# Performance work log

Measured on AMD Instinct MI355X. Metric: run time of the kernel, lower is better.

The kernel has to match this reference:

```python
import jax, jax.numpy as jnp
import numpy as np
from jax import lax

E = 1e-13            # WENO smoothness epsilon
MULT_BIAS = 0.1      # weno5_mult_bias
PADS = (2, 2, 0, 0, 1, 0)


def _conv1d(x, w, b, pad):
    # x: [1, Cin, N], w: [Cout, Cin, K], b: [Cout]
    y = lax.conv_general_dilated(x, w, window_strides=(1,), padding=[(pad, pad)],
                                 dimension_numbers=('NCH', 'OIH', 'NCH'))
    return y + b[None, :, None]


def _cnn(dif, params):
    # inner_nn_weno5: 5 Conv+ELU blocks then Conv+Sigmoid; dif: [N]
    x = dif[None, None, :]
    for i in range(6):
        x = _conv1d(x, params[2 * i], params[2 * i + 1], PADS[i])
        x = jax.nn.elu(x) if i < 5 else jax.nn.sigmoid(x)
    return x[0, 0]  # [N]


def _avg_diff(uu):
    # __get_average_diff: average of left/right forward differences, edges replicated
    d = uu[1:] - uu[:-1]                       # [N-1]
    d_left = jnp.concatenate([d, d[-1:]])      # [N]
    d_right = jnp.concatenate([d[:1], d])      # [N]
    return 0.5 * (d_left + d_right)


def _weno5(uu, params):
    # w5_minus=True, mweno=True, mapped=False, trainable=True
    def fluxes(u):
        um, umm = jnp.roll(u, 1), jnp.roll(u, 2)
        up, upp = jnp.roll(u, -1), jnp.roll(u, -2)
        f0 = (11 * u - 7 * up + 2 * upp) / 6
        f1 = (2 * um + 5 * u - up) / 6
        f2 = (-umm + 5 * um + 2 * u) / 6
        return f0, f1, f2

    def betas(u):
        um, umm = jnp.roll(u, 1), jnp.roll(u, 2)
        up, upp = jnp.roll(u, -1), jnp.roll(u, -2)
        b0 = 13 / 12 * (u - 2 * up + upp) ** 2 + 0.25 * (3 * u - 4 * up + upp) ** 2
        b1 = 13 / 12 * (um - 2 * u + up) ** 2 + 0.25 * (um - up) ** 2
        b2 = 13 / 12 * (umm - 2 * um + u) ** 2 + 0.25 * (umm - 4 * um + 3 * u) ** 2
        return b0, b1, b2

    u_right = jnp.roll(uu, -1)
    fp = fluxes(u_right)
    fn = fluxes(uu)
    bp = list(betas(u_right))
    bn = list(betas(uu))

    # trainable beta correction from the small CNN flux limiter
    bm = _cnn(_avg_diff(uu), params) + MULT_BIAS
    bp = [b * jnp.roll(bm, k - 1) for k, b in enumerate(bp)]
    bn = [b * jnp.roll(bm, k - 1) for k, b in enumerate(bn)]

    ds = (0.1, 0.6, 0.3)

    def omegas(bs):  # mweno=True variant, then normalize
        brs = (bs[2] - bs[0]) ** 2
        om = [d / (E + b) ** 2 * (brs + (E + b) ** 2) for b, d in zip(bs, ds)]
        s = om[0] + om[1] + om[2]
        return [o / s for o in om]

    op = omegas(bp)
    on = omegas(bn)
    fluxp = op[0] * fp[0] + op[1] * fp[1] + op[2] * fp[2]
    fluxn = on[0] * fn[0] + on[1] * fn[1] + on[2] * fn[2]
    return fluxp - fluxn


def setup_inputs() -> dict:
    key = jax.random.key(0)
    ks = jax.random.split(key, 13)
    N = 2097152
    uu = jax.random.normal(ks[0], (N,), dtype=jnp.float32)
    shapes = [(20, 1, 5), (40, 20, 5), (80, 40, 1), (40, 80, 1), (20, 40, 3), (1, 20, 1)]
    inp = {'uu': uu}
    for i, (co, ci, k) in enumerate(shapes):
        fan_in = ci * k
        scale = jnp.float32(1.0 / np.sqrt(fan_in))
        inp[f'w{i + 1}'] = jax.random.normal(ks[2 * i + 1], (co, ci, k), dtype=jnp.float32) * scale
        inp[f'b{i + 1}'] = jax.random.normal(ks[2 * i + 2], (co,), dtype=jnp.float32) * 0.01
    return inp


def reference(uu, w1, b1, w2, b2, w3, b3, w4, b4, w5, b5, w6, b6):
    params = (w1, b1, w2, b2, w3, b3, w4, b4, w5, b5, w6, b6)
    return _weno5(uu, params)
```

## Files before the change

kernel.cpp:

```cpp
#include <hip/hip_runtime.h>
#include <cstdint>

#define N_PTS 2097152
#define MASK  (N_PTS - 1)

constexpr int NPOS = 128;
constexpr int POUT = 116;
constexpr int GOFF = 6;
constexpr int BLK  = 256;
constexpr int NBLK = (N_PTS + POUT - 1) / POUT;

constexpr int ST1 = 40;
constexpr int ST2 = 72;
constexpr int ST3 = 104;
constexpr int ST4 = 72;

constexpr int SLOTA_OFF = 0;
constexpr int SLOTA_SZ  = 128 * ST3 * 2;
constexpr int SLOTB_OFF = SLOTA_SZ;
constexpr int SLOTB_SZ  = 130 * ST4 * 2;
constexpr int TAIL_OFF  = SLOTB_OFF + SLOTB_SZ;
constexpr int SMEM_BYTES = TAIL_OFF + 392 * 4;

constexpr int F2 = 0;
constexpr int F3 = 7680;
constexpr int F4 = 12800;
constexpr int F5 = 17408;
constexpr int F1 = 23552;
constexpr int NFRAG2 = 15, NFRAG3 = 10, NFRAG4 = 9, NFRAG5 = 12;
constexpr int NPREP = NFRAG2 + NFRAG3 + NFRAG4 + NFRAG5 + 2;
constexpr int BME_OFF = 65536;

typedef __bf16 bf16x8 __attribute__((ext_vector_type(8)));
typedef unsigned short u16x8 __attribute__((ext_vector_type(8)));
typedef float f32x4 __attribute__((ext_vector_type(4)));

constexpr unsigned short BF16_ONE = 0x3F80;

__device__ __forceinline__ float elu(float x) { return x > 0.f ? x : __expf(x) - 1.f; }

__device__ __forceinline__ float fastrcp(float x) {
#if __has_builtin(__builtin_amdgcn_rcpf)
    return __builtin_amdgcn_rcpf(x);
#else
    return 1.f / x;
#endif
}

__device__ __forceinline__ unsigned short f2b_rtne(float f) {
    union { float f; unsigned int u; } x; x.f = f;
    return (unsigned short)((x.u + 0x7fffu + ((x.u >> 16) & 1u)) >> 16);
}
__device__ __forceinline__ unsigned int pack_bf16_2(float lo, float hi) {
#if __has_builtin(__builtin_amdgcn_perm)
    union { float f; unsigned int u; } a, b;
    a.f = lo; b.f = hi;
    return __builtin_amdgcn_perm(b.u + 0x8000u, a.u + 0x8000u, 0x07060302u);
#else
    union { float f; unsigned int u; } a, b;
    a.f = lo; b.f = hi;
    return ((a.u + 0x8000u) >> 16) | (((b.u + 0x8000u) >> 16) << 16);
#endif
}

template<int M, int MT, int CI, int KS, int KT>
__device__ __forceinline__ void pack_one(const float* __restrict__ W,
                                         const float* __restrict__ Bias, int biasTap,
                                         unsigned short* __restrict__ dst,
                                         int f, int lane)
{
    const int ks = f % KS;
    const int fi = f / KS;
    const int mt = fi % MT;
    const int t  = fi / MT;
    const int m  = mt * 16 + (lane & 15);
    const int kb = ks * 32 + (lane >> 4) * 8;
    u16x8 v;
    #pragma unroll
    for (int j = 0; j < 8; ++j) {
        const int k = kb + j;
        float val = 0.f;
        if (m < M) {
            if (k < CI)                          val = W[(m * CI + k) * KT + t];
            else if (k == CI && t == biasTap)    val = Bias[m];
        }
        v[j] = f2b_rtne(val);
    }
    *(u16x8*)(dst + (f * 64 + lane) * 8) = v;
}

__global__ __launch_bounds__(64) void prep_kernel(
    const float* __restrict__ w1, const float* __restrict__ b1,
    const float* __restrict__ w2, const float* __restrict__ b2,
    const float* __restrict__ w3, const float* __restrict__ b3,
    const float* __restrict__ w4, const float* __restrict__ b4,
    const float* __restrict__ w5, const float* __restrict__ b5,
    unsigned short* __restrict__ frags)
{
    const int lane = threadIdx.x;
    const int b = blockIdx.x;
    if (b < NFRAG2)
        pack_one<40, 3, 20, 1, 5>(w2, b2, 2, frags + F2, b, lane);
    else if (b < NFRAG2 + NFRAG3)
        pack_one<80, 5, 40, 2, 1>(w3, b3, 0, frags + F3, b - NFRAG2, lane);
    else if (b < NFRAG2 + NFRAG3 + NFRAG4)
        pack_one<40, 3, 80, 3, 1>(w4, b4, 0, frags + F4, b - NFRAG2 - NFRAG3, lane);
    else if (b < NFRAG2 + NFRAG3 + NFRAG4 + NFRAG5)
        pack_one<20, 2, 40, 2, 3>(w5, b5, 1, frags + F5, b - NFRAG2 - NFRAG3 - NFRAG4, lane);
    else {
        const int mt = b - (NPREP - 2);
        const int m  = mt * 16 + (lane & 15);
        const int kb = (lane >> 4) * 8;
        u16x8 v;
        #pragma unroll
        for (int j = 0; j < 8; ++j) {
            const int k = kb + j;
            float val = 0.f;
            if (m < 20) {
                if (k < 5)      val = w1[m * 5 + k];
                else if (k == 5) val = b1[m];
            }
            v[j] = f2b_rtne(val);
        }
        *(u16x8*)(frags + F1 + (mt * 64 + lane) * 8) = v;
    }
}

template<int TAPS, int MT, int KS, typename Epi>
__device__ __forceinline__ void gemm_tap(const unsigned short* __restrict__ Af,
                                         const unsigned short* __restrict__ Bbuf,
                                         int SB, Epi epi)
{
    const int lane = threadIdx.x & 63;
    const int wv   = threadIdx.x >> 6;
    const int n15  = lane & 15;
    const int quad = lane >> 4;

    bf16x8 A[TAPS * MT * KS];
    #pragma unroll
    for (int f = 0; f < TAPS * MT * KS; ++f)
        A[f] = __builtin_bit_cast(bf16x8, *(const u16x8*)(Af + (f * 64 + lane) * 8));

    #pragma unroll
    for (int nt = 0; nt < 2; ++nt) {
        const int pos = (wv * 2 + nt) * 16 + n15;
        bf16x8 B[TAPS][KS];
        #pragma unroll
        for (int t = 0; t < TAPS; ++t)
            #pragma unroll
            for (int ks = 0; ks < KS; ++ks)
                B[t][ks] = __builtin_bit_cast(bf16x8,
                    *(const u16x8*)(Bbuf + (pos + t) * SB + ks * 32 + quad * 8));
        #pragma unroll
        for (int mt = 0; mt < MT; ++mt) {
            f32x4 acc = {0.f, 0.f, 0.f, 0.f};
            #pragma unroll
            for (int t = 0; t < TAPS; ++t)
                #pragma unroll
                for (int ks = 0; ks < KS; ++ks)
                    acc = __builtin_amdgcn_mfma_f32_16x16x32_bf16(
                        A[(t * MT + mt) * KS + ks], B[t][ks], acc, 0, 0, 0);
            epi(mt, pos, acc);
        }
    }
}

__device__ __forceinline__ float weno_math(float um2, float um1, float u0,
                                           float up1, float up2, float up3,
                                           float bmm, float bm0, float bmp)
{
    const float c1312 = 13.f / 12.f;
    const float s6 = 1.f / 6.f;

    const float f0p = (11.f * up1 - 7.f * up2 + 2.f * up3) * s6;
    const float f1p = (2.f * u0 + 5.f * up1 - up2) * s6;
    const float f2p = (-um1 + 5.f * u0 + 2.f * up1) * s6;
    const float f0n = (11.f * u0 - 7.f * up1 + 2.f * up2) * s6;
    const float f1n = (2.f * um1 + 5.f * u0 - up1) * s6;
    const float f2n = (-um2 + 5.f * um1 + 2.f * u0) * s6;

    float t0, t1;
    t0 = up1 - 2.f * up2 + up3;  t1 = 3.f * up1 - 4.f * up2 + up3;
    float bp0 = c1312 * t0 * t0 + 0.25f * t1 * t1;
    t0 = u0 - 2.f * up1 + up2;   t1 = u0 - up2;
    float bp1 = c1312 * t0 * t0 + 0.25f * t1 * t1;
    t0 = um1 - 2.f * u0 + up1;   t1 = um1 - 4.f * u0 + 3.f * up1;
    float bp2 = c1312 * t0 * t0 + 0.25f * t1 * t1;
    t0 = u0 - 2.f * up1 + up2;   t1 = 3.f * u0 - 4.f * up1 + up2;
    float bn0 = c1312 * t0 * t0 + 0.25f * t1 * t1;
    t0 = um1 - 2.f * u0 + up1;   t1 = um1 - up1;
    float bn1 = c1312 * t0 * t0 + 0.25f * t1 * t1;
    t0 = um2 - 2.f * um1 + u0;   t1 = um2 - 4.f * um1 + 3.f * u0;
    float bn2 = c1312 * t0 * t0 + 0.25f * t1 * t1;

    bp0 *= bmp; bp1 *= bm0; bp2 *= bmm;
    bn0 *= bmp; bn1 *= bm0; bn2 *= bmm;

    const float E = 1e-13f;
    float brs, e, r0, r1, r2, o0, o1, o2;

    brs = bp2 - bp0; brs *= brs;
    e = E + bp0; e *= e; r0 = fastrcp(e);
    e = E + bp1; e *= e; r1 = fastrcp(e);
    e = E + bp2; e *= e; r2 = fastrcp(e);
    o0 = 0.1f * fmaf(brs, r0, 1.f);
    o1 = 0.6f * fmaf(brs, r1, 1.f);
    o2 = 0.3f * fmaf(brs, r2, 1.f);
    const float fluxp = (o0 * f0p + o1 * f1p + o2 * f2p) * fastrcp(o0 + o1 + o2);

    brs = bn2 - bn0; brs *= brs;
    e = E + bn0; e *= e; r0 = fastrcp(e);
    e = E + bn1; e *= e; r1 = fastrcp(e);
    e = E + bn2; e *= e; r2 = fastrcp(e);
    o0 = 0.1f * fmaf(brs, r0, 1.f);
    o1 = 0.6f * fmaf(brs, r1, 1.f);
    o2 = 0.3f * fmaf(brs, r2, 1.f);
    const float fluxn = (o0 * f0n + o1 * f1n + o2 * f2n) * fastrcp(o0 + o1 + o2);

    return fluxp - fluxn;
}

__global__ __launch_bounds__(BLK, 3) void cnn_weno_kernel(
    const float* __restrict__ u,
    const float* __restrict__ w6, const float* __restrict__ b6,
    const unsigned short* __restrict__ frags,
    float* __restrict__ bmE,
    float* __restrict__ out)
{
    extern __shared__ char smem[];
    unsigned short* act1 = (unsigned short*)(smem + SLOTA_OFF);
    unsigned short* act3 = (unsigned short*)(smem + SLOTA_OFF);
    unsigned short* act2 = (unsigned short*)(smem + SLOTB_OFF);
    unsigned short* act4 = (unsigned short*)(smem + SLOTB_OFF);
    float* sdif = (float*)(smem + TAIL_OFF);
    float* sw6  = sdif + 132;
    float* sb6  = sw6 + 20;
    float* sbm  = sb6 + 1;
    float* su   = sbm + 118;

    const int tid  = threadIdx.x;
    const int lane = tid & 63;
    const int wv   = tid >> 6;
    const int n15  = lane & 15;
    const int quad = lane >> 4;
    const int i0   = blockIdx.x * POUT;
    const bool edge = (blockIdx.x == 0) || (blockIdx.x >= NBLK - 1);

    {
        const u16x8 z8 = {0, 0, 0, 0, 0, 0, 0, 0};
        for (int i = tid; i < 130 * 2; i += BLK) {
            const int r = i >> 1, c = 48 + (i & 1) * 8;
            *(u16x8*)(act2 + r * ST2 + c) = z8;
        }
        for (int i = tid; i < 128 * 2; i += BLK) {
            const int r = i >> 1, j = i & 1;
            u16x8 v = {0, 0, 0, 0, 0, 0, 0, 0};
            if (j == 0) v[0] = BF16_ONE;
            *(u16x8*)(act3 + r * ST3 + 80 + j * 8) = v;
        }
    }
    for (int d = tid; d < 132; d += BLK) {
        const int g = i0 - 10 + d;
        float v = 0.f;
        if (g >= 0 && g < N_PTS) {
            if (g == 0)              v = u[1] - u[0];
            else if (g == N_PTS - 1) v = u[N_PTS - 1] - u[N_PTS - 2];
            else                     v = 0.5f * (u[g + 1] - u[g - 1]);
        }
        sdif[d] = v;
    }
    for (int j = tid; j < 121; j += BLK)
        su[j] = u[(i0 - 2 + j) & MASK];
    if (tid < 20)       sw6[tid] = w6[tid];
    else if (tid == 20) sb6[0] = b6[0];
    __syncthreads();

    {
        bf16x8 A1[2];
        #pragma unroll
        for (int f = 0; f < 2; ++f)
            A1[f] = __builtin_bit_cast(bf16x8,
                *(const u16x8*)(frags + F1 + (f * 64 + lane) * 8));
        #pragma unroll
        for (int nt = 0; nt < 2; ++nt) {
            const int pos = (wv * 2 + nt) * 16 + n15;
            const float s0 = sdif[pos],     s1 = sdif[pos + 1], s2 = sdif[pos + 2],
                        s3 = sdif[pos + 3], s4 = sdif[pos + 4];
            uint4 bd;
            bd.x = pack_bf16_2(s0, s1);
            bd.y = pack_bf16_2(s2, s3);
            bd.z = pack_bf16_2(s4, 1.0f);
            bd.w = 0u;
            const bf16x8 B = __builtin_bit_cast(bf16x8, bd);
            const f32x4 z = {0.f, 0.f, 0.f, 0.f};
            const f32x4 a0 = __builtin_amdgcn_mfma_f32_16x16x32_bf16(A1[0], B, z, 0, 0, 0);
            const f32x4 a1 = __builtin_amdgcn_mfma_f32_16x16x32_bf16(A1[1], B, z, 0, 0, 0);
            bool oor = false;
            if (edge) {
                const int g = i0 + pos - 8;
                oor = ((unsigned)g >= (unsigned)N_PTS);
            }
            {
                float v0 = elu(a0[0]), v1 = elu(a0[1]), v2 = elu(a0[2]), v3 = elu(a0[3]);
                if (oor) { v0 = v1 = v2 = v3 = 0.f; }
                uint2 w; w.x = pack_bf16_2(v0, v1); w.y = pack_bf16_2(v2, v3);
                *(uint2*)(act1 + pos * ST1 + quad * 4) = w;
            }
            {
                uint2 w;
                if (quad == 0) {
                    float v0 = elu(a1[0]), v1 = elu(a1[1]), v2 = elu(a1[2]), v3 = elu(a1[3]);
                    if (oor) { v0 = v1 = v2 = v3 = 0.f; }
                    w.x = pack_bf16_2(v0, v1); w.y = pack_bf16_2(v2, v3);
                } else if (quad == 1) {
                    w.x = (unsigned)BF16_ONE; w.y = 0u;
                } else {
                    w.x = 0u; w.y = 0u;
                }
                *(uint2*)(act1 + pos * ST1 + 16 + quad * 4) = w;
            }
        }
    }
    __syncthreads();

    gemm_tap<5, 3, 1>(frags + F2, act1, ST1,
        [&](int mt, int pos, f32x4 acc) {
            const int ch0 = mt * 16 + quad * 4;
            unsigned short* dst = act2 + pos * ST2 + ch0;
            if (mt < 2 || quad < 2) {
                float v0 = elu(acc[0]), v1 = elu(acc[1]), v2 = elu(acc[2]), v3 = elu(acc[3]);
                if (edge) {
                    const int g = i0 - GOFF + pos;
                    if ((unsigned)g >= (unsigned)N_PTS) { v0 = v1 = v2 = v3 = 0.f; }
                }
                uint2 w; w.x = pack_bf16_2(v0, v1); w.y = pack_bf16_2(v2, v3);
                *(uint2*)dst = w;
            } else {
                uint2 w; w.x = (quad == 2) ? (unsigned)BF16_ONE : 0u; w.y = 0u;
                *(uint2*)dst = w;
            }
        });
    __syncthreads();

    gemm_tap<1, 5, 2>(frags + F3, act2, ST2,
        [&](int mt, int pos, f32x4 acc) {
            const int ch0 = mt * 16 + quad * 4;
            float v0 = elu(acc[0]), v1 = elu(acc[1]), v2 = elu(acc[2]), v3 = elu(acc[3]);
            if (edge) {
                const int g = i0 - GOFF + pos;
                if ((unsigned)g >= (unsigned)N_PTS) { v0 = v1 = v2 = v3 = 0.f; }
            }
            uint2 w; w.x = pack_bf16_2(v0, v1); w.y = pack_bf16_2(v2, v3);
            *(uint2*)(act3 + pos * ST3 + ch0) = w;
        });
    __syncthreads();

    gemm_tap<1, 3, 3>(frags + F4, act3, ST3,
        [&](int mt, int pos, f32x4 acc) {
            const int ch0 = mt * 16 + quad * 4;
            unsigned short* dst = act4 + (pos + 1) * ST4 + ch0;
            if (mt < 2 || quad < 2) {
                float v0 = elu(acc[0]), v1 = elu(acc[1]), v2 = elu(acc[2]), v3 = elu(acc[3]);
                if (edge) {
                    const int g = i0 - GOFF + pos;
                    if ((unsigned)g >= (unsigned)N_PTS) { v0 = v1 = v2 = v3 = 0.f; }
                }
                uint2 w; w.x = pack_bf16_2(v0, v1); w.y = pack_bf16_2(v2, v3);
                *(uint2*)dst = w;
            } else {
                uint2 w; w.x = (quad == 2) ? (unsigned)BF16_ONE : 0u; w.y = 0u;
                *(uint2*)dst = w;
            }
        });
    __syncthreads();

    {
        const unsigned short* Af = frags + F5;
        bf16x8 A5[12];
        #pragma unroll
        for (int f = 0; f < 12; ++f)
            A5[f] = __builtin_bit_cast(bf16x8, *(const u16x8*)(Af + (f * 64 + lane) * 8));

        #pragma unroll
        for (int nt = 0; nt < 2; ++nt) {
            const int pos = (wv * 2 + nt) * 16 + n15;
            bf16x8 B[3][2];
            #pragma unroll
            for (int t = 0; t < 3; ++t)
                #pragma unroll
                for (int ks = 0; ks < 2; ++ks)
                    B[t][ks] = __builtin_bit_cast(bf16x8,
                        *(const u16x8*)(act4 + (pos + t) * ST4 + ks * 32 + quad * 8));
            f32x4 a0 = {0.f, 0.f, 0.f, 0.f};
            f32x4 a1 = {0.f, 0.f, 0.f, 0.f};
            #pragma unroll
            for (int t = 0; t < 3; ++t)
                #pragma unroll
                for (int ks = 0; ks < 2; ++ks) {
                    a0 = __builtin_amdgcn_mfma_f32_16x16x32_bf16(
                        A5[(t * 2 + 0) * 2 + ks], B[t][ks], a0, 0, 0, 0);
                    a1 = __builtin_amdgcn_mfma_f32_16x16x32_bf16(
                        A5[(t * 2 + 1) * 2 + ks], B[t][ks], a1, 0, 0, 0);
                }
            float partial = 0.f;
            const int c0 = quad * 4;
            #pragma unroll
            for (int r = 0; r < 4; ++r)
                partial += sw6[c0 + r] * elu(a0[r]);
            if (quad == 0) {
                #pragma unroll
                for (int r = 0; r < 4; ++r)
                    partial += sw6[16 + r] * elu(a1[r]);
            }
            partial += __shfl_xor(partial, 16, 64);
            partial += __shfl_xor(partial, 32, 64);
            if (quad == 0) {
                const float bmv = fastrcp(1.f + __expf(-(partial + sb6[0]))) + 0.1f;
                if (pos >= 5 && pos < 123) sbm[pos - 5] = bmv;
                if (edge) {
                    const int g = i0 - GOFF + pos;
                    if (blockIdx.x == 0) {
                        if (g == 0) bmE[0] = bmv;
                        else if (g == 1) bmE[1] = bmv;
                    }
                    if (blockIdx.x == NBLK - 1) {
                        if (g == N_PTS - 2) bmE[2] = bmv;
                        else if (g == N_PTS - 1) bmE[3] = bmv;
                    }
                }
            }
        }
    }
    __syncthreads();

    if (tid < POUT) {
        const int g = i0 + tid;
        if (g < N_PTS && g != 0 && g != N_PTS - 1) {
            out[g] = weno_math(su[tid], su[tid + 1], su[tid + 2],
                               su[tid + 3], su[tid + 4], su[tid + 5],
                               sbm[tid], sbm[tid + 1], sbm[tid + 2]);
        }
    }
}

__global__ __launch_bounds__(64) void patch_kernel(
    const float* __restrict__ u, const float* __restrict__ bmE,
    float* __restrict__ out)
{
    const int t = threadIdx.x;
    if (t < 2) {
        const int g = (t == 0) ? 0 : (N_PTS - 1);
        const float bmm = (t == 0) ? bmE[3] : bmE[2];
        const float bm0 = (t == 0) ? bmE[0] : bmE[3];
        const float bmp = (t == 0) ? bmE[1] : bmE[0];
        out[g] = weno_math(u[(g - 2) & MASK], u[(g - 1) & MASK], u[g],
                           u[(g + 1) & MASK], u[(g + 2) & MASK], u[(g + 3) & MASK],
                           bmm, bm0, bmp);
    }
}

extern "C" void kernel_launch(void* const* d_in, const int* in_sizes, int n_in,
                              void* d_out, int out_size, void* d_ws, size_t ws_size,
                              hipStream_t stream) {
    const float* u  = (const float*)d_in[0];
    const float* w1 = (const float*)d_in[1];
    const float* b1 = (const float*)d_in[2];
    const float* w2 = (const float*)d_in[3];
    const float* b2 = (const float*)d_in[4];
    const float* w3 = (const float*)d_in[5];
    const float* b3 = (const float*)d_in[6];
    const float* w4 = (const float*)d_in[7];
    const float* b4 = (const float*)d_in[8];
    const float* w5 = (const float*)d_in[9];
    const float* b5 = (const float*)d_in[10];
    const float* w6 = (const float*)d_in[11];
    const float* b6 = (const float*)d_in[12];

    unsigned short* frags = (unsigned short*)d_ws;
    float* bmE = (float*)((char*)d_ws + BME_OFF);

    (void)hipFuncSetAttribute((const void*)cnn_weno_kernel,
                              hipFuncAttributeMaxDynamicSharedMemorySize,
                              SMEM_BYTES);

    prep_kernel<<<NPREP, 64, 0, stream>>>(w1, b1, w2, b2, w3, b3, w4, b4, w5, b5, frags);
    cnn_weno_kernel<<<NBLK, BLK, SMEM_BYTES, stream>>>(u, w6, b6, frags, bmE,
                                                       (float*)d_out);
    patch_kernel<<<1, 64, 0, stream>>>(u, bmE, (float*)d_out);
}
```

Baseline: 299.4 us.

## Fold edge patch into main kernel via last-block atomic counter

Removes the separate patch kernel launch: each block bumps a global counter after finishing, and the last block computes the two periodic edge outputs from the stored boundary bm values. It also splits the halo loading into a fast path without bounds checks for interior blocks, and seeds each MFMA accumulation chain with a shared zero vector instead of a fresh zero initialiser. The exchange is one extra atomic and a __syncthreads per block, plus a __threadfence on the edge writers.

```diff
diff --git a/kernel.cpp b/kernel.cpp
--- a/kernel.cpp
+++ b/kernel.cpp
@@ -95,10 +95,12 @@
     const float* __restrict__ w3, const float* __restrict__ b3,
     const float* __restrict__ w4, const float* __restrict__ b4,
     const float* __restrict__ w5, const float* __restrict__ b5,
-    unsigned short* __restrict__ frags)
+    unsigned short* __restrict__ frags,
+    unsigned int* __restrict__ counter)
 {
     const int lane = threadIdx.x;
     const int b = blockIdx.x;
+    if (b == 0 && lane == 0) counter[0] = 0u;
     if (b < NFRAG2)
         pack_one<40, 3, 20, 1, 5>(w2, b2, 2, frags + F2, b, lane);
     else if (b < NFRAG2 + NFRAG3)
@@ -129,7 +131,7 @@
 template<int TAPS, int MT, int KS, typename Epi>
 __device__ __forceinline__ void gemm_tap(const unsigned short* __restrict__ Af,
                                          const unsigned short* __restrict__ Bbuf,
-                                         int SB, Epi epi)
+                                         int SB, f32x4 Z4, Epi epi)
 {
     const int lane = threadIdx.x & 63;
     const int wv   = threadIdx.x >> 6;
@@ -153,13 +155,14 @@
                     *(const u16x8*)(Bbuf + (pos + t) * SB + ks * 32 + quad * 8));
         #pragma unroll
         for (int mt = 0; mt < MT; ++mt) {
-            f32x4 acc = {0.f, 0.f, 0.f, 0.f};
+            f32x4 acc = __builtin_amdgcn_mfma_f32_16x16x32_bf16(
+                A[mt * KS], B[0][0], Z4, 0, 0, 0);
             #pragma unroll
-            for (int t = 0; t < TAPS; ++t)
-                #pragma unroll
-                for (int ks = 0; ks < KS; ++ks)
-                    acc = __builtin_amdgcn_mfma_f32_16x16x32_bf16(
-                        A[(t * MT + mt) * KS + ks], B[t][ks], acc, 0, 0, 0);
+            for (int i = 1; i < TAPS * KS; ++i) {
+                const int t = i / KS, ks = i - t * KS;
+                acc = __builtin_amdgcn_mfma_f32_16x16x32_bf16(
+                    A[(t * MT + mt) * KS + ks], B[t][ks], acc, 0, 0, 0);
+            }
             epi(mt, pos, acc);
         }
     }
@@ -225,6 +228,7 @@
     const float* __restrict__ w6, const float* __restrict__ b6,
     const unsigned short* __restrict__ frags,
     float* __restrict__ bmE,
+    unsigned int* __restrict__ counter,
     float* __restrict__ out)
 {
     extern __shared__ char smem[];
@@ -246,6 +250,8 @@
     const int i0   = blockIdx.x * POUT;
     const bool edge = (blockIdx.x == 0) || (blockIdx.x >= NBLK - 1);
 
+    const f32x4 Z4 = {0.f, 0.f, 0.f, 0.f};
+
     {
         const u16x8 z8 = {0, 0, 0, 0, 0, 0, 0, 0};
         for (int i = tid; i < 130 * 2; i += BLK) {
@@ -259,18 +265,27 @@
             *(u16x8*)(act3 + r * ST3 + 80 + j * 8) = v;
         }
     }
-    for (int d = tid; d < 132; d += BLK) {
-        const int g = i0 - 10 + d;
-        float v = 0.f;
-        if (g >= 0 && g < N_PTS) {
-            if (g == 0)              v = u[1] - u[0];
-            else if (g == N_PTS - 1) v = u[N_PTS - 1] - u[N_PTS - 2];
-            else                     v = 0.5f * (u[g + 1] - u[g - 1]);
-        }
-        sdif[d] = v;
-    }
-    for (int j = tid; j < 121; j += BLK)
-        su[j] = u[(i0 - 2 + j) & MASK];
+    if (!edge) {
+        for (int d = tid; d < 132; d += BLK) {
+            const int g = i0 - 10 + d;
+            sdif[d] = 0.5f * (u[g + 1] - u[g - 1]);
+        }
+        for (int j = tid; j < 121; j += BLK)
+            su[j] = u[i0 - 2 + j];
+    } else {
+        for (int d = tid; d < 132; d += BLK) {
+            const int g = i0 - 10 + d;
+            float v = 0.f;
+            if (g >= 0 && g < N_PTS) {
+                if (g == 0)              v = u[1] - u[0];
+                else if (g == N_PTS - 1) v = u[N_PTS - 1] - u[N_PTS - 2];
+                else                     v = 0.5f * (u[g + 1] - u[g - 1]);
+            }
+            sdif[d] = v;
+        }
+        for (int j = tid; j < 121; j += BLK)
+            su[j] = u[(i0 - 2 + j) & MASK];
+    }
     if (tid < 20)       sw6[tid] = w6[tid];
     else if (tid == 20) sb6[0] = b6[0];
     __syncthreads();
@@ -292,9 +307,8 @@
             bd.z = pack_bf16_2(s4, 1.0f);
             bd.w = 0u;
             const bf16x8 B = __builtin_bit_cast(bf16x8, bd);
-            const f32x4 z = {0.f, 0.f, 0.f, 0.f};
-            const f32x4 a0 = __builtin_amdgcn_mfma_f32_16x16x32_bf16(A1[0], B, z, 0, 0, 0);
-            const f32x4 a1 = __builtin_amdgcn_mfma_f32_16x16x32_bf16(A1[1], B, z, 0, 0, 0);
+            const f32x4 a0 = __builtin_amdgcn_mfma_f32_16x16x32_bf16(A1[0], B, Z4, 0, 0, 0);
+            const f32x4 a1 = __builtin_amdgcn_mfma_f32_16x16x32_bf16(A1[1], B, Z4, 0, 0, 0);
             bool oor = false;
             if (edge) {
                 const int g = i0 + pos - 8;
@@ -323,7 +337,7 @@
     }
     __syncthreads();
 
-    gemm_tap<5, 3, 1>(frags + F2, act1, ST1,
+    gemm_tap<5, 3, 1>(frags + F2, act1, ST1, Z4,
         [&](int mt, int pos, f32x4 acc) {
             const int ch0 = mt * 16 + quad * 4;
             unsigned short* dst = act2 + pos * ST2 + ch0;
@@ -342,7 +356,7 @@
         });
     __syncthreads();
 
-    gemm_tap<1, 5, 2>(frags + F3, act2, ST2,
+    gemm_tap<1, 5, 2>(frags + F3, act2, ST2, Z4,
         [&](int mt, int pos, f32x4 acc) {
             const int ch0 = mt * 16 + quad * 4;
             float v0 = elu(acc[0]), v1 = elu(acc[1]), v2 = elu(acc[2]), v3 = elu(acc[3]);
@@ -355,7 +369,7 @@
         });
     __syncthreads();
 
-    gemm_tap<1, 3, 3>(frags + F4, act3, ST3,
+    gemm_tap<1, 3, 3>(frags + F4, act3, ST3, Z4,
         [&](int mt, int pos, f32x4 acc) {
             const int ch0 = mt * 16 + quad * 4;
             unsigned short* dst = act4 + (pos + 1) * ST4 + ch0;
@@ -391,17 +405,16 @@
                 for (int ks = 0; ks < 2; ++ks)
                     B[t][ks] = __builtin_bit_cast(bf16x8,
                         *(const u16x8*)(act4 + (pos + t) * ST4 + ks * 32 + quad * 8));
-            f32x4 a0 = {0.f, 0.f, 0.f, 0.f};
-            f32x4 a1 = {0.f, 0.f, 0.f, 0.f};
+            f32x4 a0 = __builtin_amdgcn_mfma_f32_16x16x32_bf16(A5[0], B[0][0], Z4, 0, 0, 0);
+            f32x4 a1 = __builtin_amdgcn_mfma_f32_16x16x32_bf16(A5[2], B[0][0], Z4, 0, 0, 0);
             #pragma unroll
-            for (int t = 0; t < 3; ++t)
-                #pragma unroll
-                for (int ks = 0; ks < 2; ++ks) {
-                    a0 = __builtin_amdgcn_mfma_f32_16x16x32_bf16(
-                        A5[(t * 2 + 0) * 2 + ks], B[t][ks], a0, 0, 0, 0);
-                    a1 = __builtin_amdgcn_mfma_f32_16x16x32_bf16(
-                        A5[(t * 2 + 1) * 2 + ks], B[t][ks], a1, 0, 0, 0);
-                }
+            for (int i = 1; i < 6; ++i) {
+                const int t = i >> 1, ks = i & 1;
+                a0 = __builtin_amdgcn_mfma_f32_16x16x32_bf16(
+                    A5[(t * 2 + 0) * 2 + ks], B[t][ks], a0, 0, 0, 0);
+                a1 = __builtin_amdgcn_mfma_f32_16x16x32_bf16(
+                    A5[(t * 2 + 1) * 2 + ks], B[t][ks], a1, 0, 0, 0);
+            }
             float partial = 0.f;
             const int c0 = quad * 4;
             #pragma unroll
@@ -419,14 +432,16 @@
                 if (pos >= 5 && pos < 123) sbm[pos - 5] = bmv;
                 if (edge) {
                     const int g = i0 - GOFF + pos;
+                    bool wrote = false;
                     if (blockIdx.x == 0) {
-                        if (g == 0) bmE[0] = bmv;
-                        else if (g == 1) bmE[1] = bmv;
+                        if (g == 0)      { bmE[0] = bmv; wrote = true; }
+                        else if (g == 1) { bmE[1] = bmv; wrote = true; }
                     }
                     if (blockIdx.x == NBLK - 1) {
-                        if (g == N_PTS - 2) bmE[2] = bmv;
-                        else if (g == N_PTS - 1) bmE[3] = bmv;
+                        if (g == N_PTS - 2)      { bmE[2] = bmv; wrote = true; }
+                        else if (g == N_PTS - 1) { bmE[3] = bmv; wrote = true; }
                     }
+                    if (wrote) __threadfence();
                 }
             }
         }
@@ -441,21 +456,19 @@
                                sbm[tid], sbm[tid + 1], sbm[tid + 2]);
         }
     }
-}
-
-__global__ __launch_bounds__(64) void patch_kernel(
-    const float* __restrict__ u, const float* __restrict__ bmE,
-    float* __restrict__ out)
-{
-    const int t = threadIdx.x;
-    if (t < 2) {
-        const int g = (t == 0) ? 0 : (N_PTS - 1);
-        const float bmm = (t == 0) ? bmE[3] : bmE[2];
-        const float bm0 = (t == 0) ? bmE[0] : bmE[3];
-        const float bmp = (t == 0) ? bmE[1] : bmE[0];
-        out[g] = weno_math(u[(g - 2) & MASK], u[(g - 1) & MASK], u[g],
-                           u[(g + 1) & MASK], u[(g + 2) & MASK], u[(g + 3) & MASK],
-                           bmm, bm0, bmp);
+
+    __syncthreads();
+    if (tid == 0) {
+        const unsigned int old = atomicAdd(counter, 1u);
+        if (old == (unsigned int)(NBLK - 1)) {
+            __threadfence();
+            volatile const float* vb = bmE;
+            const float b0 = vb[0], b1 = vb[1], b2 = vb[2], b3 = vb[3];
+            out[0] = weno_math(u[N_PTS - 2], u[N_PTS - 1], u[0],
+                               u[1], u[2], u[3], b3, b0, b1);
+            out[N_PTS - 1] = weno_math(u[N_PTS - 3], u[N_PTS - 2], u[N_PTS - 1],
+                                       u[0], u[1], u[2], b2, b3, b0);
+        }
     }
 }
 
@@ -478,13 +491,14 @@
 
     unsigned short* frags = (unsigned short*)d_ws;
     float* bmE = (float*)((char*)d_ws + BME_OFF);
+    unsigned int* counter = (unsigned int*)((char*)d_ws + BME_OFF + 16);
 
     (void)hipFuncSetAttribute((const void*)cnn_weno_kernel,
                               hipFuncAttributeMaxDynamicSharedMemorySize,
                               SMEM_BYTES);
 
-    prep_kernel<<<NPREP, 64, 0, stream>>>(w1, b1, w2, b2, w3, b3, w4, b4, w5, b5, frags);
+    prep_kernel<<<NPREP, 64, 0, stream>>>(w1, b1, w2, b2, w3, b3, w4, b4, w5, b5,
+                                          frags, counter);
     cnn_weno_kernel<<<NBLK, BLK, SMEM_BYTES, stream>>>(u, w6, b6, frags, bmE,
-                                                       (float*)d_out);
-    patch_kernel<<<1, 64, 0, stream>>>(u, bmE, (float*)d_out);
-}
+                                                       counter, (float*)d_out);
+}
```

After: 310.6 us. +3.7%, slower.
